# Performance work log

Hardware: AMD Instinct MI355X
Metric: run time of the kernel (lower is better)

Reference implementation:

```python
import jax, jax.numpy as jnp
import numpy as np

DIM = 256; DIM_HEAD = 32; HEADS = DIM // DIM_HEAD; WSZ = 8; D4 = DIM // 4
EPS = 1e-5
SCALE = DIM_HEAD ** -0.5


def _rel_pos_indices(wsz):
    pos = np.arange(wsz)
    grid = np.stack(np.meshgrid(pos, pos, indexing='ij')).reshape(2, -1).T  # (w*w, 2)
    rel = grid[:, None] - grid[None, :] + wsz - 1
    return jnp.asarray((rel * np.array([2 * wsz - 1, 1])).sum(-1))  # (w*w, w*w)


def _ln(x, g, b):
    m = x.mean(-1, keepdims=True)
    v = jnp.var(x, axis=-1, keepdims=True)
    return (x - m) / jnp.sqrt(v + EPS) * g + b


def setup_inputs() -> dict:
    key = jax.random.key(0)
    ks = jax.random.split(key, 8)
    inner = HEADS * DIM_HEAD
    def n(k, shape, s=0.02):
        return jax.random.normal(k, shape, dtype=jnp.float32) * s
    return {
        "x": jax.random.normal(ks[0], (2, DIM, 256, 256), dtype=jnp.float32),
        "norm_g": jnp.ones((1, DIM, 1, 1), jnp.float32),
        "norm_b": jnp.zeros((1, DIM, 1, 1), jnp.float32),
        "w_qkv": n(ks[1], (3 * inner, DIM)),
        "w_out": n(ks[2], (DIM, inner)),
        "b_out": jnp.zeros((DIM,), jnp.float32),
        "dpb_w1": n(ks[3], (D4, 2), 0.5), "dpb_b1": jnp.zeros((D4,), jnp.float32),
        "dpb_g1": jnp.ones((D4,), jnp.float32), "dpb_beta1": jnp.zeros((D4,), jnp.float32),
        "dpb_w2": n(ks[4], (D4, D4), 0.1), "dpb_b2": jnp.zeros((D4,), jnp.float32),
        "dpb_g2": jnp.ones((D4,), jnp.float32), "dpb_beta2": jnp.zeros((D4,), jnp.float32),
        "dpb_w3": n(ks[5], (D4, D4), 0.1), "dpb_b3": jnp.zeros((D4,), jnp.float32),
        "dpb_g3": jnp.ones((D4,), jnp.float32), "dpb_beta3": jnp.zeros((D4,), jnp.float32),
        "dpb_w4": n(ks[6], (1, D4), 0.1), "dpb_b4": jnp.zeros((1,), jnp.float32),
    }


def reference(x, norm_g, norm_b, w_qkv, w_out, b_out,
              dpb_w1, dpb_b1, dpb_g1, dpb_beta1,
              dpb_w2, dpb_b2, dpb_g2, dpb_beta2,
              dpb_w3, dpb_b3, dpb_g3, dpb_beta3,
              dpb_w4, dpb_b4):
    B, D, H, W = x.shape
    nh, nw = H // WSZ, W // WSZ
    # channel-first LayerNorm (stats over dim=1, biased variance)
    mean = x.mean(axis=1, keepdims=True)
    var = jnp.var(x, axis=1, keepdims=True)
    xn = (x - mean) / jnp.sqrt(var + EPS) * norm_g + norm_b
    # 'short' windowing: b d (h s1) (w s2) -> (b h w) d (s1 s2)
    xw = xn.reshape(B, D, nh, WSZ, nw, WSZ).transpose(0, 2, 4, 1, 3, 5)
    xw = xw.reshape(B * nh * nw, D, WSZ * WSZ)
    # 1x1 conv QKV == matmul over channel dim
    qkv = jnp.einsum('ed,bdn->ben', w_qkv, xw)
    q, k, v = jnp.split(qkv, 3, axis=1)
    to_heads = lambda t: t.reshape(-1, HEADS, DIM_HEAD, WSZ * WSZ).transpose(0, 1, 3, 2)
    q, k, v = to_heads(q) * SCALE, to_heads(k), to_heads(v)
    sim = jnp.einsum('bhid,bhjd->bhij', q, k)  # [Bw, H, 64, 64]
    # dynamic position bias MLP over relative coordinates in [-wsz, wsz]
    pos = jnp.arange(-WSZ, WSZ + 1, dtype=x.dtype)
    rel = jnp.stack(jnp.meshgrid(pos, pos, indexing='ij')).reshape(2, -1).T  # ((2w+1)^2, 2)
    h1 = jax.nn.relu(_ln(rel @ dpb_w1.T + dpb_b1, dpb_g1, dpb_beta1))
    h2 = jax.nn.relu(_ln(h1 @ dpb_w2.T + dpb_b2, dpb_g2, dpb_beta2))
    h3 = jax.nn.relu(_ln(h2 @ dpb_w3.T + dpb_b3, dpb_g3, dpb_beta3))
    biases = (h3 @ dpb_w4.T + dpb_b4)[:, 0]
    sim = sim + biases[_rel_pos_indices(WSZ)]
    attn = jax.nn.softmax(sim, axis=-1)
    out = jnp.einsum('bhij,bhjd->bhid', attn, v)
    # b h (x y) d -> b (h d) (x y)
    out = out.transpose(0, 1, 3, 2).reshape(-1, HEADS * DIM_HEAD, WSZ * WSZ)
    out = jnp.einsum('de,ben->bdn', w_out, out) + b_out[None, :, None]
    # (b h w) d s1 s2 -> b d (h s1) (w s2)
    out = out.reshape(B, nh, nw, D, WSZ, WSZ).transpose(0, 3, 1, 4, 2, 5).reshape(B, D, H, W)
    return out
```

## Files before the change

### kernel.cpp

```cpp
#include <hip/hip_runtime.h>


typedef __attribute__((ext_vector_type(8))) short bf16x8;
typedef __attribute__((ext_vector_type(4))) short bf16x4;
typedef __attribute__((ext_vector_type(4))) float f32x4;

#define LOG2E    1.44269504088896f
#define QK_SCALE 0.17677669529663687f

__device__ __forceinline__ short f2b(float f) {
  union { float f; unsigned u; } v; v.f = f;
  unsigned r = v.u + 0x7FFFu + ((v.u >> 16) & 1u);
  return (short)(r >> 16);
}

__device__ __forceinline__ unsigned pk2(float a, float b) {
  union { float f; unsigned u; } ua, ub; ua.f = a; ub.f = b;
#if __has_builtin(__builtin_amdgcn_perm)
  return __builtin_amdgcn_perm(ub.u + 0x8000u, ua.u + 0x8000u, 0x07060302u);
#else
  return ((ua.u + 0x8000u) >> 16) | ((ub.u + 0x8000u) & 0xFFFF0000u);
#endif
}

__device__ __forceinline__ bf16x8 mk8(unsigned a, unsigned b, unsigned c, unsigned d) {
  union { unsigned u[4]; bf16x8 v; } x; x.u[0] = a; x.u[1] = b; x.u[2] = c; x.u[3] = d;
  return x.v;
}
__device__ __forceinline__ bf16x4 mk4(unsigned a, unsigned b) {
  union { unsigned u[2]; bf16x4 v; } x; x.u[0] = a; x.u[1] = b; return x.v;
}

__device__ __forceinline__ f32x4 mfma16(bf16x4 a, bf16x4 b, f32x4 c) {
#if __has_builtin(__builtin_amdgcn_mfma_f32_16x16x16bf16_1k)
  return __builtin_amdgcn_mfma_f32_16x16x16bf16_1k(a, b, c, 0, 0, 0);
#else
  f32x4 d;
  asm volatile("v_mfma_f32_16x16x16_bf16 %0, %1, %2, %3"
               : "=&v"(d) : "v"(a), "v"(b), "v"(c));
  return d;
#endif
}

__device__ __forceinline__ float wave_sum64(float v) {
  v += __shfl_xor(v, 1);  v += __shfl_xor(v, 2);  v += __shfl_xor(v, 4);
  v += __shfl_xor(v, 8);  v += __shfl_xor(v, 16); v += __shfl_xor(v, 32);
  return v;
}

__global__ __launch_bounds__(256)
void prep_kernel(const float* __restrict__ wqkv, const float* __restrict__ wout,
                 const float* __restrict__ w1, const float* __restrict__ b1,
                 const float* __restrict__ g1, const float* __restrict__ be1,
                 const float* __restrict__ w2, const float* __restrict__ b2,
                 const float* __restrict__ g2, const float* __restrict__ be2,
                 const float* __restrict__ w3, const float* __restrict__ b3,
                 const float* __restrict__ g3, const float* __restrict__ be3,
                 const float* __restrict__ w4, const float* __restrict__ b4,
                 short* __restrict__ wq_t, short* __restrict__ wo_t,
                 float* __restrict__ sb) {
  __shared__ float h[64];
  __shared__ float wbuf[4096];

  if (blockIdx.x < 128) {
    int t = (blockIdx.x * 256 + threadIdx.x) * 8;
    if (t < 196608) {
      int blk = t >> 9, l = (t & 511) >> 3;
      int et = blk >> 3, kt = blk & 7;
      int e = et * 16 + (l & 15);
      int d = kt * 32 + (l >> 4) * 8;
      const float* src = wqkv + e * 256 + d;
      float sc = (e < 256) ? QK_SCALE * LOG2E : 1.0f;
      bf16x8 pk;
      #pragma unroll
      for (int el = 0; el < 8; ++el) pk[el] = f2b(src[el] * sc);
      *(bf16x8*)(wq_t + t) = pk;
    } else {
      int o = t - 196608;
      int blk = o >> 9, l = (o & 511) >> 3;
      int dt = blk >> 3, kt = blk & 7;
      int dout = dt * 16 + (l & 15);
      int e = kt * 32 + (l >> 4) * 8;
      const float* src = wout + dout * 256 + e;
      bf16x8 pk;
      #pragma unroll
      for (int el = 0; el < 8; ++el) pk[el] = f2b(src[el]);
      *(bf16x8*)(wo_t + o) = pk;
    }
    return;
  }

  if (threadIdx.x >= 64) return;
  const int f = threadIdx.x;
  const int pos = blockIdx.x - 128;
  const float py = (float)(pos / 17) - 8.0f;
  const float px = (float)(pos % 17) - 8.0f;

  float a = py * w1[2 * f] + px * w1[2 * f + 1] + b1[f];
  {
    float m = wave_sum64(a) * (1.f / 64.f);
    float d = a - m;
    float var = wave_sum64(d * d) * (1.f / 64.f);
    a = fmaxf(d * rsqrtf(var + 1e-5f) * g1[f] + be1[f], 0.f);
  }
  h[f] = a;
  __threadfence_block();

  #pragma unroll 8
  for (int k = 0; k < 64; ++k) wbuf[k * 64 + f] = w2[k * 64 + f];
  __threadfence_block();
  float acc = b2[f];
  #pragma unroll 8
  for (int k = 0; k < 64; ++k) {
    int g = (k + f) & 63;
    acc += wbuf[f * 64 + g] * h[g];
  }
  {
    float m = wave_sum64(acc) * (1.f / 64.f);
    float d = acc - m;
    float var = wave_sum64(d * d) * (1.f / 64.f);
    acc = fmaxf(d * rsqrtf(var + 1e-5f) * g2[f] + be2[f], 0.f);
  }
  __threadfence_block();
  h[f] = acc;
  __threadfence_block();

  #pragma unroll 8
  for (int k = 0; k < 64; ++k) wbuf[k * 64 + f] = w3[k * 64 + f];
  __threadfence_block();
  float acc3 = b3[f];
  #pragma unroll 8
  for (int k = 0; k < 64; ++k) {
    int g = (k + f) & 63;
    acc3 += wbuf[f * 64 + g] * h[g];
  }
  {
    float m = wave_sum64(acc3) * (1.f / 64.f);
    float d = acc3 - m;
    float var = wave_sum64(d * d) * (1.f / 64.f);
    acc3 = fmaxf(d * rsqrtf(var + 1e-5f) * g3[f] + be3[f], 0.f);
  }
  float o = wave_sum64(w4[f] * acc3);
  if (f == 0) sb[pos] = o + b4[0];
}

__global__ __launch_bounds__(512)
void expand_kernel(const float* __restrict__ sb, float* __restrict__ tblf) {
  int idx = blockIdx.x * 512 + threadIdx.x;
  int it = idx >> 10, jt = (idx >> 8) & 3, ln = (idx >> 2) & 63, jj = idx & 3;
  int rr = ln & 15, gg = ln >> 4;
  int i = it * 16 + rr;
  int j = jt * 16 + gg * 4 + jj;
  int dy = (i >> 3) - (j >> 3) + 7;
  int dx = (i & 7) - (j & 7) + 7;
  tblf[idx] = sb[dy * 15 + dx] * LOG2E;
}

#define SM_XA   0
#define SM_PS   65536
#define SM_SIZE 73728
#define XASWZ(p) ((((p) & 7) << 4) ^ ((((p) >> 3) & 3) << 7))

__global__ __launch_bounds__(512)
void attn_kernel(const float* __restrict__ x, const float* __restrict__ gnorm,
                 const float* __restrict__ bnorm, const short* __restrict__ wq_t,
                 const short* __restrict__ wo_t, const float* __restrict__ bout,
                 const float* __restrict__ tblf, float* __restrict__ out) {
  __shared__ __align__(16) char smem[SM_SIZE];
  const int t = threadIdx.x;
  const int lane = t & 63;
  const int w = t >> 6;
  const int r = lane & 15;
  const int gq = lane >> 4;

  const int bid = blockIdx.x;
  const int b   = bid >> 9;
  const int wh  = (bid >> 4) & 31;
  const int ww2 = bid & 15;
  const int R = wh * 8, C = ww2 * 16;

  const int n = lane;
  const int d0 = w * 32;
  float* PS = (float*)(smem + SM_PS);
  float xv[2][32];
  #pragma unroll
  for (int h = 0; h < 2; ++h) {
    const float* xb = x + (((size_t)(b * 256 + d0)) << 16) +
                      (R + 4 * h + (n >> 4)) * 256 + C + (n & 15);
    float s1 = 0.f, s2v = 0.f;
    #pragma unroll
    for (int i = 0; i < 32; ++i) {
      float v = xb[(size_t)i << 16];
      xv[h][i] = v; s1 += v; s2v += v * v;
    }
    PS[h * 1024 + w * 64 + n] = s1;
    PS[h * 1024 + 512 + w * 64 + n] = s2v;
  }
  __syncthreads();
  #pragma unroll
  for (int h = 0; h < 2; ++h) {
    float a = 0.f, q2 = 0.f;
    #pragma unroll
    for (int dg = 0; dg < 8; ++dg) {
      a  += PS[h * 1024 + dg * 64 + n];
      q2 += PS[h * 1024 + 512 + dg * 64 + n];
    }
    float mean = a * (1.f / 256.f);
    float var = q2 * (1.f / 256.f) - mean * mean;
    float rstd = rsqrtf(var + 1e-5f);
    int p2 = (4 * h + (n >> 4)) * 16 + (n & 15);
    #pragma unroll
    for (int c = 0; c < 4; ++c) {
      float xn[8];
      #pragma unroll
      for (int e = 0; e < 8; ++e) {
        int d = d0 + c * 8 + e;
        xn[e] = (xv[h][c * 8 + e] - mean) * rstd * gnorm[d] + bnorm[d];
      }
      *(bf16x8*)(smem + SM_XA + (p2 << 9) + ((((d0 + c * 8) << 1)) ^ XASWZ(p2))) =
          mk8(pk2(xn[0], xn[1]), pk2(xn[2], xn[3]), pk2(xn[4], xn[5]), pk2(xn[6], xn[7]));
    }
  }
  __syncthreads();

  const f32x4 vzero = {0.f, 0.f, 0.f, 0.f};

  f32x4 o2[2][2][4];
  float pinv[2][4];
  #pragma unroll
  for (int wl = 0; wl < 2; ++wl) {
    bf16x4 kpk[2][4], qpk[2][4];
    {
      f32x4 aq[2][4], ak[2][4];
      #pragma unroll
      for (int nt = 0; nt < 2; ++nt)
        #pragma unroll
        for (int t4 = 0; t4 < 4; ++t4) { aq[nt][t4] = vzero; ak[nt][t4] = vzero; }
      #pragma unroll
      for (int kt = 0; kt < 8; ++kt) {
        bf16x8 bq0 = *(const bf16x8*)(wq_t + ((((0 * 16 + w * 2 + 0) * 8 + kt) << 9) + lane * 8));
        bf16x8 bq1 = *(const bf16x8*)(wq_t + ((((0 * 16 + w * 2 + 1) * 8 + kt) << 9) + lane * 8));
        bf16x8 bk0 = *(const bf16x8*)(wq_t + ((((1 * 16 + w * 2 + 0) * 8 + kt) << 9) + lane * 8));
        bf16x8 bk1 = *(const bf16x8*)(wq_t + ((((1 * 16 + w * 2 + 1) * 8 + kt) << 9) + lane * 8));
        bf16x8 afr[4];
        #pragma unroll
        for (int t4 = 0; t4 < 4; ++t4) {
          int p2 = (t4 * 2 + (r >> 3)) * 16 + wl * 8 + (r & 7);
          afr[t4] = *(const bf16x8*)(smem + SM_XA + (p2 << 9) + ((((kt * 32 + gq * 8) << 1)) ^ XASWZ(p2)));
        }
        #pragma unroll
        for (int t4 = 0; t4 < 4; ++t4) {
          aq[0][t4] = __builtin_amdgcn_mfma_f32_16x16x32_bf16(bq0, afr[t4], aq[0][t4], 0, 0, 0);
          aq[1][t4] = __builtin_amdgcn_mfma_f32_16x16x32_bf16(bq1, afr[t4], aq[1][t4], 0, 0, 0);
          ak[0][t4] = __builtin_amdgcn_mfma_f32_16x16x32_bf16(bk0, afr[t4], ak[0][t4], 0, 0, 0);
          ak[1][t4] = __builtin_amdgcn_mfma_f32_16x16x32_bf16(bk1, afr[t4], ak[1][t4], 0, 0, 0);
        }
      }
      #pragma unroll
      for (int kb = 0; kb < 2; ++kb)
        #pragma unroll
        for (int t4 = 0; t4 < 4; ++t4) {
          qpk[kb][t4] = mk4(pk2(aq[kb][t4][0], aq[kb][t4][1]),
                            pk2(aq[kb][t4][2], aq[kb][t4][3]));
          kpk[kb][t4] = mk4(pk2(ak[kb][t4][0], ak[kb][t4][1]),
                            pk2(ak[kb][t4][2], ak[kb][t4][3]));
        }
    }
    bf16x4 va8[4][2];
    {
      f32x4 vacc[4][2];
      #pragma unroll
      for (int mt = 0; mt < 4; ++mt)
        #pragma unroll
        for (int nt = 0; nt < 2; ++nt) vacc[mt][nt] = vzero;
      #pragma unroll
      for (int kt = 0; kt < 8; ++kt) {
        bf16x8 bfr0 = *(const bf16x8*)(wq_t + ((((2 * 16 + w * 2 + 0) * 8 + kt) << 9) + lane * 8));
        bf16x8 bfr1 = *(const bf16x8*)(wq_t + ((((2 * 16 + w * 2 + 1) * 8 + kt) << 9) + lane * 8));
        bf16x8 afr[4];
        #pragma unroll
        for (int mt = 0; mt < 4; ++mt) {
          int p2 = (mt * 2 + (r >> 3)) * 16 + wl * 8 + (r & 7);
          afr[mt] = *(const bf16x8*)(smem + SM_XA + (p2 << 9) + ((((kt * 32 + gq * 8) << 1)) ^ XASWZ(p2)));
        }
        #pragma unroll
        for (int mt = 0; mt < 4; ++mt) {
          vacc[mt][0] = __builtin_amdgcn_mfma_f32_16x16x32_bf16(afr[mt], bfr0, vacc[mt][0], 0, 0, 0);
          vacc[mt][1] = __builtin_amdgcn_mfma_f32_16x16x32_bf16(afr[mt], bfr1, vacc[mt][1], 0, 0, 0);
        }
      }
      #pragma unroll
      for (int mt = 0; mt < 4; ++mt)
        #pragma unroll
        for (int nt = 0; nt < 2; ++nt)
          va8[mt][nt] = mk4(pk2(vacc[mt][nt][0], vacc[mt][nt][1]),
                            pk2(vacc[mt][nt][2], vacc[mt][nt][3]));
    }

    #pragma unroll
    for (int nt = 0; nt < 2; ++nt)
      #pragma unroll
      for (int it = 0; it < 4; ++it) o2[wl][nt][it] = vzero;
    __builtin_amdgcn_s_setprio(1);
    #pragma unroll
    for (int it = 0; it < 4; ++it) {
      f32x4 sc[4];
      #pragma unroll
      for (int jt = 0; jt < 4; ++jt) {
        sc[jt] = mfma16(kpk[0][jt], qpk[0][it], vzero);
        sc[jt] = mfma16(kpk[1][jt], qpk[1][it], sc[jt]);
      }
      float sum = 0.f;
      #pragma unroll
      for (int jt = 0; jt < 4; ++jt) {
        f32x4 bj = *(const f32x4*)(tblf + (((it * 4 + jt) * 64 + lane) << 2));
        #pragma unroll
        for (int jj = 0; jj < 4; ++jj) {
          float e = exp2f(sc[jt][jj] + bj[jj]);
          sc[jt][jj] = e; sum += e;
        }
      }
      sum += __shfl_xor(sum, 16);
      sum += __shfl_xor(sum, 32);
      pinv[wl][it] = 1.0f / sum;
      bf16x4 ppk[4];
      #pragma unroll
      for (int jt = 0; jt < 4; ++jt)
        ppk[jt] = mk4(pk2(sc[jt][0], sc[jt][1]), pk2(sc[jt][2], sc[jt][3]));
      #pragma unroll
      for (int mt = 0; mt < 4; ++mt)
        #pragma unroll
        for (int nt = 0; nt < 2; ++nt)
          o2[wl][nt][it] = mfma16(va8[mt][nt], ppk[mt], o2[wl][nt][it]);
    }
    __builtin_amdgcn_s_setprio(0);
  }
  __syncthreads();

  #pragma unroll
  for (int wl = 0; wl < 2; ++wl)
    #pragma unroll
    for (int nt = 0; nt < 2; ++nt)
      #pragma unroll
      for (int it = 0; it < 4; ++it) {
        float pv = pinv[wl][it];
        int pw = it * 16 + r;
        int p2 = ((pw >> 3) << 4) + (wl << 3) + (pw & 7);
        int e = (w << 5) + (nt << 4) + (gq << 2);
        *(bf16x4*)(smem + SM_XA + (p2 << 9) + (((e << 1)) ^ XASWZ(p2))) =
            mk4(pk2(o2[wl][nt][it][0] * pv, o2[wl][nt][it][1] * pv),
                pk2(o2[wl][nt][it][2] * pv, o2[wl][nt][it][3] * pv));
      }
  __syncthreads();

  float bov[2];
  bov[0] = bout[w * 32 + r];
  bov[1] = bout[w * 32 + 16 + r];
  bf16x8 woB[2][8];
  #pragma unroll
  for (int nt = 0; nt < 2; ++nt)
    #pragma unroll
    for (int kt = 0; kt < 8; ++kt)
      woB[nt][kt] = *(const bf16x8*)(wo_t + ((((w * 2 + nt) * 8 + kt) << 9) + lane * 8));

  #pragma unroll 1
  for (int ck = 0; ck < 2; ++ck) {
    f32x4 c3[4][2];
    #pragma unroll
    for (int mt = 0; mt < 4; ++mt)
      #pragma unroll
      for (int nt = 0; nt < 2; ++nt) c3[mt][nt] = vzero;
    __builtin_amdgcn_s_setprio(1);
    #pragma unroll
    for (int kt = 0; kt < 8; ++kt) {
      bf16x8 af[4];
      #pragma unroll
      for (int mt = 0; mt < 4; ++mt) {
        int p2 = ck * 64 + mt * 16 + r;
        af[mt] = *(const bf16x8*)(smem + SM_XA + (p2 << 9) + ((((kt * 32 + gq * 8) << 1)) ^ XASWZ(p2)));
      }
      #pragma unroll
      for (int mt = 0; mt < 4; ++mt)
        #pragma unroll
        for (int nt = 0; nt < 2; ++nt)
          c3[mt][nt] = __builtin_amdgcn_mfma_f32_16x16x32_bf16(af[mt], woB[nt][kt], c3[mt][nt], 0, 0, 0);
    }
    __builtin_amdgcn_s_setprio(0);
    #pragma unroll
    for (int mt = 0; mt < 4; ++mt)
      #pragma unroll
      for (int nt = 0; nt < 2; ++nt) {
        int dout = w * 32 + nt * 16 + r;
        int row = ck * 4 + mt;
        f32x4 v = c3[mt][nt];
        v[0] += bov[nt]; v[1] += bov[nt]; v[2] += bov[nt]; v[3] += bov[nt];
        *(f32x4*)(out + (((size_t)(b * 256 + dout)) << 16) + (R + row) * 256 + C + gq * 4) = v;
      }
  }
}

extern "C" void kernel_launch(void* const* d_in, const int* in_sizes, int n_in,
                              void* d_out, int out_size, void* d_ws, size_t ws_size,
                              hipStream_t stream) {
  const float* x     = (const float*)d_in[0];
  const float* gnorm = (const float*)d_in[1];
  const float* bnorm = (const float*)d_in[2];
  const float* wqkv  = (const float*)d_in[3];
  const float* wout  = (const float*)d_in[4];
  const float* bout  = (const float*)d_in[5];
  const float* w1  = (const float*)d_in[6];
  const float* b1  = (const float*)d_in[7];
  const float* g1  = (const float*)d_in[8];
  const float* be1 = (const float*)d_in[9];
  const float* w2  = (const float*)d_in[10];
  const float* b2  = (const float*)d_in[11];
  const float* g2  = (const float*)d_in[12];
  const float* be2 = (const float*)d_in[13];
  const float* w3  = (const float*)d_in[14];
  const float* b3  = (const float*)d_in[15];
  const float* g3  = (const float*)d_in[16];
  const float* be3 = (const float*)d_in[17];
  const float* w4  = (const float*)d_in[18];
  const float* b4  = (const float*)d_in[19];

  short* wq_t = (short*)d_ws;
  short* wo_t = wq_t + 196608;
  float* sb   = (float*)((char*)d_ws + 524288);
  float* tblf = (float*)((char*)d_ws + 528384);

  prep_kernel<<<dim3(417), dim3(256), 0, stream>>>(
      wqkv, wout, w1, b1, g1, be1, w2, b2, g2, be2, w3, b3, g3, be3, w4, b4,
      wq_t, wo_t, sb);
  expand_kernel<<<dim3(8), dim3(512), 0, stream>>>(sb, tblf);

  attn_kernel<<<dim3(1024), dim3(512), 0, stream>>>(
      x, gnorm, bnorm, wq_t, wo_t, bout, tblf, (float*)d_out);
}
```

Measured before the change: 177.7 us.

## Precompute per-pixel LayerNorm statistics in a separate kernel

Adds a stats kernel that computes per-pixel channel mean and rstd over x and stores them in workspace. The attention kernel then loads these stats instead of reducing partial sums through shared memory and a block barrier. This shrinks shared memory and removes one sync, at the cost of an extra full read of the input tensor and an extra launch.

```diff
diff --git a/kernel.cpp b/kernel.cpp
--- a/kernel.cpp
+++ b/kernel.cpp
@@ -46,6 +46,25 @@
   v += __shfl_xor(v, 1);  v += __shfl_xor(v, 2);  v += __shfl_xor(v, 4);
   v += __shfl_xor(v, 8);  v += __shfl_xor(v, 16); v += __shfl_xor(v, 32);
   return v;
+}
+
+__global__ __launch_bounds__(256)
+void stats_kernel(const float* __restrict__ x, float* __restrict__ statsb) {
+  const int j = threadIdx.x;
+  const int h = blockIdx.x & 255;
+  const int b = blockIdx.x >> 8;
+  const float* xp = x + ((size_t)b << 24) + (h << 8) + j;
+  float s1 = 0.f, s2 = 0.f;
+  #pragma unroll 16
+  for (int d = 0; d < 256; ++d) {
+    float v = xp[(size_t)d << 16];
+    s1 += v; s2 += v * v;
+  }
+  float mean = s1 * (1.f / 256.f);
+  float var = s2 * (1.f / 256.f) - mean * mean;
+  int pix = (b << 16) + (h << 8) + j;
+  statsb[pix] = mean;
+  statsb[131072 + pix] = rsqrtf(var + 1e-5f);
 }
 
 __global__ __launch_bounds__(256)
@@ -157,15 +176,15 @@
 }
 
 #define SM_XA   0
-#define SM_PS   65536
-#define SM_SIZE 73728
+#define SM_SIZE 65536
 #define XASWZ(p) ((((p) & 7) << 4) ^ ((((p) >> 3) & 3) << 7))
 
 __global__ __launch_bounds__(512)
-void attn_kernel(const float* __restrict__ x, const float* __restrict__ gnorm,
-                 const float* __restrict__ bnorm, const short* __restrict__ wq_t,
-                 const short* __restrict__ wo_t, const float* __restrict__ bout,
-                 const float* __restrict__ tblf, float* __restrict__ out) {
+void attn_kernel(const float* __restrict__ x, const float* __restrict__ statsb,
+                 const short* __restrict__ wq_t, const short* __restrict__ wo_t,
+                 const float* __restrict__ gnorm, const float* __restrict__ bnorm,
+                 const float* __restrict__ bout, const float* __restrict__ tblf,
+                 float* __restrict__ out) {
   __shared__ __align__(16) char smem[SM_SIZE];
   const int t = threadIdx.x;
   const int lane = t & 63;
@@ -181,33 +200,17 @@
 
   const int n = lane;
   const int d0 = w * 32;
-  float* PS = (float*)(smem + SM_PS);
-  float xv[2][32];
   #pragma unroll
   for (int h = 0; h < 2; ++h) {
-    const float* xb = x + (((size_t)(b * 256 + d0)) << 16) +
-                      (R + 4 * h + (n >> 4)) * 256 + C + (n & 15);
-    float s1 = 0.f, s2v = 0.f;
-    #pragma unroll
-    for (int i = 0; i < 32; ++i) {
-      float v = xb[(size_t)i << 16];
-      xv[h][i] = v; s1 += v; s2v += v * v;
-    }
-    PS[h * 1024 + w * 64 + n] = s1;
-    PS[h * 1024 + 512 + w * 64 + n] = s2v;
-  }
-  __syncthreads();
-  #pragma unroll
-  for (int h = 0; h < 2; ++h) {
-    float a = 0.f, q2 = 0.f;
-    #pragma unroll
-    for (int dg = 0; dg < 8; ++dg) {
-      a  += PS[h * 1024 + dg * 64 + n];
-      q2 += PS[h * 1024 + 512 + dg * 64 + n];
-    }
-    float mean = a * (1.f / 256.f);
-    float var = q2 * (1.f / 256.f) - mean * mean;
-    float rstd = rsqrtf(var + 1e-5f);
+    const int row = R + 4 * h + (n >> 4);
+    const int col = C + (n & 15);
+    const float* xb = x + (((size_t)(b * 256 + d0)) << 16) + row * 256 + col;
+    float xv[32];
+    #pragma unroll
+    for (int i = 0; i < 32; ++i) xv[i] = xb[(size_t)i << 16];
+    int pix = (b << 16) + row * 256 + col;
+    float mean = statsb[pix];
+    float rstd = statsb[131072 + pix];
     int p2 = (4 * h + (n >> 4)) * 16 + (n & 15);
     #pragma unroll
     for (int c = 0; c < 4; ++c) {
@@ -215,7 +218,7 @@
       #pragma unroll
       for (int e = 0; e < 8; ++e) {
         int d = d0 + c * 8 + e;
-        xn[e] = (xv[h][c * 8 + e] - mean) * rstd * gnorm[d] + bnorm[d];
+        xn[e] = (xv[c * 8 + e] - mean) * rstd * gnorm[d] + bnorm[d];
       }
       *(bf16x8*)(smem + SM_XA + (p2 << 9) + ((((d0 + c * 8) << 1)) ^ XASWZ(p2))) =
           mk8(pk2(xn[0], xn[1]), pk2(xn[2], xn[3]), pk2(xn[4], xn[5]), pk2(xn[6], xn[7]));
@@ -423,16 +426,18 @@
   const float* w4  = (const float*)d_in[18];
   const float* b4  = (const float*)d_in[19];
 
-  short* wq_t = (short*)d_ws;
-  short* wo_t = wq_t + 196608;
-  float* sb   = (float*)((char*)d_ws + 524288);
-  float* tblf = (float*)((char*)d_ws + 528384);
-
+  short* wq_t   = (short*)d_ws;
+  short* wo_t   = wq_t + 196608;
+  float* sb     = (float*)((char*)d_ws + 524288);
+  float* tblf   = (float*)((char*)d_ws + 528384);
+  float* statsb = (float*)((char*)d_ws + 544768);
+
+  stats_kernel<<<dim3(512), dim3(256), 0, stream>>>(x, statsb);
   prep_kernel<<<dim3(417), dim3(256), 0, stream>>>(
       wqkv, wout, w1, b1, g1, be1, w2, b2, g2, be2, w3, b3, g3, be3, w4, b4,
       wq_t, wo_t, sb);
   expand_kernel<<<dim3(8), dim3(512), 0, stream>>>(sb, tblf);
 
   attn_kernel<<<dim3(1024), dim3(512), 0, stream>>>(
-      x, gnorm, bnorm, wq_t, wo_t, bout, tblf, (float*)d_out);
-}
+      x, statsb, wq_t, wo_t, gnorm, bnorm, bout, tblf, (float*)d_out);
+}
```

Result: slower. 184.9 us (+4.0%).
